# Performance work log

Hardware: AMD Instinct MI355X
Metric: run time of the kernel (lower is better)

The kernel has to match this reference:

```python
import jax, jax.numpy as jnp
import numpy as np

EPS = 1e-6
DN = ('NCHW', 'OIHW', 'NCHW')


def _dw_conv(s, w, dilation, k):
    pad = dilation * (k - 1) // 2
    return jax.lax.conv_general_dilated(
        s, w, window_strides=(1, 1), padding=[(pad, pad), (pad, pad)],
        rhs_dilation=(dilation, dilation), dimension_numbers=DN,
        feature_group_count=4)


def _branch(s, dw_w, pw_w, pw_b, dilation, k):
    h = _dw_conv(s, dw_w, dilation, k)           # [B,4,H,W]
    # pointwise 1x1 conv 4 -> 1
    return jnp.einsum('bchw,oc->bohw', h, pw_w) + pw_b[None, :, None, None]


def setup_inputs() -> dict:
    key = jax.random.key(0)
    ks = jax.random.split(key, 12)
    B, C, H, W = 32, 64, 128, 128
    nb, rh = 3, 8
    d = {}
    d['x'] = jax.random.normal(ks[0], (B, C, H, W), dtype=jnp.float32)
    # branch 0: k=3 d=1; branch 1: k=7 d=1; branch 2: k=7 d=2
    d['dw0'] = jax.random.normal(ks[1], (4, 1, 3, 3), dtype=jnp.float32) * 0.2
    d['dw1'] = jax.random.normal(ks[2], (4, 1, 7, 7), dtype=jnp.float32) * 0.1
    d['dw2'] = jax.random.normal(ks[3], (4, 1, 7, 7), dtype=jnp.float32) * 0.1
    d['pw0_w'] = jax.random.normal(ks[4], (1, 4), dtype=jnp.float32) * 0.5
    d['pw0_b'] = jnp.zeros((1,), dtype=jnp.float32)
    d['pw1_w'] = jax.random.normal(ks[5], (1, 4), dtype=jnp.float32) * 0.5
    d['pw1_b'] = jnp.zeros((1,), dtype=jnp.float32)
    d['pw2_w'] = jax.random.normal(ks[6], (1, 4), dtype=jnp.float32) * 0.5
    d['pw2_b'] = jnp.zeros((1,), dtype=jnp.float32)
    # router: 1x1 convs on pooled [B,4,1,1] == dense layers
    d['rw1'] = jax.random.normal(ks[7], (rh, 4), dtype=jnp.float32) * 0.5
    d['rb1'] = jnp.zeros((rh,), dtype=jnp.float32)
    d['rw2'] = jax.random.normal(ks[8], (nb, rh), dtype=jnp.float32) * 0.3
    d['rb2'] = jnp.zeros((nb,), dtype=jnp.float32)
    # t_raw = softplus_inverse(1.0)
    d['t_raw'] = jnp.asarray(np.log(np.expm1(1.0)), dtype=jnp.float32)
    return d


def reference(x, dw0, dw1, dw2, pw0_w, pw0_b, pw1_w, pw1_b, pw2_w, pw2_b,
              rw1, rb1, rw2, rb2, t_raw):
    B, C, H, W = x.shape
    avg_map = jnp.mean(x, axis=1, keepdims=True)        # [B,1,H,W]
    max_map = jnp.max(x, axis=1, keepdims=True)         # [B,1,H,W]
    xs = jnp.linspace(-1.0, 1.0, W, dtype=x.dtype)
    ys = jnp.linspace(-1.0, 1.0, H, dtype=x.dtype)
    yy, xx = jnp.meshgrid(ys, xs, indexing='ij')
    xg = jnp.broadcast_to(xx[None, None], (B, 1, H, W))
    yg = jnp.broadcast_to(yy[None, None], (B, 1, H, W))
    s = jnp.concatenate([avg_map, max_map, xg, yg], axis=1)  # [B,4,H,W]

    # router: global avg pool -> 1x1 conv -> relu -> 1x1 conv -> softmax
    pooled = jnp.mean(s, axis=(2, 3))                    # [B,4]
    hid = jax.nn.relu(pooled @ rw1.T + rb1)              # [B,rh]
    logits = hid @ rw2.T + rb2                           # [B,nb]
    rw = jax.nn.softmax(logits, axis=1)                  # [B,nb]

    z = jnp.stack([
        _branch(s, dw0, pw0_w, pw0_b, 1, 3),
        _branch(s, dw1, pw1_w, pw1_b, 1, 7),
        _branch(s, dw2, pw2_w, pw2_b, 2, 7),
    ], axis=1)                                           # [B,nb,1,H,W]

    wlogits = jnp.sum(rw[:, :, None, None, None] * z, axis=1)  # [B,1,H,W]
    T = jax.nn.softplus(t_raw) + EPS
    sa = jax.nn.sigmoid(wlogits / T)                     # [B,1,H,W]
    Y = x * sa                                           # [B,C,H,W]
    return (Y, sa)
```

## Files before the change

### kernel.cpp

```cpp
#include <hip/hip_runtime.h>

#define B_ 32
#define C_ 64
#define H_ 128
#define W_ 128
#define HW_ (H_*W_)
#define CHW_ (C_*HW_)

__global__ __launch_bounds__(256) void k1_reduce(
    const float* __restrict__ x, float* __restrict__ avgmap,
    float* __restrict__ maxmap, float* __restrict__ bsum)
{
    int t = blockIdx.x * 256 + threadIdx.x;
    int base = t * 4;
    int b = base >> 14;
    int q = base & (HW_ - 1);
    const float4* xp = (const float4*)(x + (size_t)b * CHW_ + q);
    float4 v = xp[0];
    float4 s = v, m = v;
    #pragma unroll 8
    for (int c = 1; c < C_; ++c) {
        float4 u = xp[c * (HW_ / 4)];
        s.x += u.x; s.y += u.y; s.z += u.z; s.w += u.w;
        m.x = fmaxf(m.x, u.x); m.y = fmaxf(m.y, u.y);
        m.z = fmaxf(m.z, u.z); m.w = fmaxf(m.w, u.w);
    }
    const float inv = 1.0f / C_;
    float4 a = make_float4(s.x * inv, s.y * inv, s.z * inv, s.w * inv);
    ((float4*)avgmap)[t] = a;
    ((float4*)maxmap)[t] = m;

    float la = a.x + a.y + a.z + a.w;
    float lm = m.x + m.y + m.z + m.w;
    #pragma unroll
    for (int o = 32; o > 0; o >>= 1) {
        la += __shfl_down(la, o);
        lm += __shfl_down(lm, o);
    }
    __shared__ float wa[4], wm[4];
    int lane = threadIdx.x & 63, wid = threadIdx.x >> 6;
    if (lane == 0) { wa[wid] = la; wm[wid] = lm; }
    __syncthreads();
    if (threadIdx.x == 0) {
        atomicAdd(&bsum[2 * b],     wa[0] + wa[1] + wa[2] + wa[3]);
        atomicAdd(&bsum[2 * b + 1], wm[0] + wm[1] + wm[2] + wm[3]);
    }
}

__global__ void k2_router(const float* __restrict__ bsum,
                          const float* __restrict__ rw1, const float* __restrict__ rb1,
                          const float* __restrict__ rw2, const float* __restrict__ rb2,
                          float* __restrict__ rwout)
{
    int b = threadIdx.x;
    if (b >= B_) return;
    float p0 = bsum[2 * b]     * (1.0f / HW_);
    float p1 = bsum[2 * b + 1] * (1.0f / HW_);
    float hid[8];
    #pragma unroll
    for (int j = 0; j < 8; ++j)
        hid[j] = fmaxf(0.0f, rb1[j] + rw1[j * 4] * p0 + rw1[j * 4 + 1] * p1);
    float lg[3];
    #pragma unroll
    for (int i = 0; i < 3; ++i) {
        float acc = rb2[i];
        #pragma unroll
        for (int j = 0; j < 8; ++j) acc += hid[j] * rw2[i * 8 + j];
        lg[i] = acc;
    }
    float mx = fmaxf(lg[0], fmaxf(lg[1], lg[2]));
    float e0 = expf(lg[0] - mx), e1 = expf(lg[1] - mx), e2 = expf(lg[2] - mx);
    float inv = 1.0f / (e0 + e1 + e2);
    rwout[b * 3 + 0] = e0 * inv;
    rwout[b * 3 + 1] = e1 * inv;
    rwout[b * 3 + 2] = e2 * inv;
}

__global__ __launch_bounds__(256) void k3_branches(
    const float* __restrict__ avgmap, const float* __restrict__ maxmap,
    const float* __restrict__ dw0, const float* __restrict__ dw1,
    const float* __restrict__ dw2,
    const float* __restrict__ pw0w, const float* __restrict__ pw0b,
    const float* __restrict__ pw1w, const float* __restrict__ pw1b,
    const float* __restrict__ pw2w, const float* __restrict__ pw2b,
    const float* __restrict__ rw, const float* __restrict__ t_raw,
    float* __restrict__ sa_out)
{
    __shared__ float sA[28][40];
    __shared__ float sM[28][40];
    __shared__ float wf0[36], wf1[196], wf2[196];

    int b = blockIdx.z;
    int tix = threadIdx.y * 16 + threadIdx.x;
    int gx0 = blockIdx.x * 16, gy0 = blockIdx.y * 16;
    const float* am = avgmap + (size_t)b * HW_;
    const float* mm = maxmap + (size_t)b * HW_;

    for (int idx = tix; idx < 28 * 28; idx += 256) {
        int r = idx / 28, c = idx % 28;
        int gy = gy0 - 6 + r, gx = gx0 - 6 + c;
        bool ok = ((unsigned)gy < H_) && ((unsigned)gx < W_);
        sA[r][c] = ok ? am[gy * W_ + gx] : 0.0f;
        sM[r][c] = ok ? mm[gy * W_ + gx] : 0.0f;
    }
    if (tix < 36)  wf0[tix] = pw0w[tix / 9]  * dw0[tix];
    if (tix < 196) {
        wf1[tix] = pw1w[tix / 49] * dw1[tix];
        wf2[tix] = pw2w[tix / 49] * dw2[tix];
    }
    __syncthreads();

    int lx = threadIdx.x, ly = threadIdx.y;
    int gx = gx0 + lx, gy = gy0 + ly;
    const float sc = 2.0f / 127.0f;

    float z0 = pw0b[0], z1 = pw1b[0], z2 = pw2b[0];

    #pragma unroll
    for (int ky = 0; ky < 3; ++ky) {
        #pragma unroll
        for (int kx = 0; kx < 3; ++kx) {
            int i = ky - 1, j = kx - 1;
            float a = sA[ly + 6 + i][lx + 6 + j];
            float m = sM[ly + 6 + i][lx + 6 + j];
            int iy = gy + i, ix = gx + j;
            bool ok = ((unsigned)iy < H_) && ((unsigned)ix < W_);
            float xv = ok ? (ix * sc - 1.0f) : 0.0f;
            float yv = ok ? (iy * sc - 1.0f) : 0.0f;
            int t = ky * 3 + kx;
            z0 += wf0[t] * a + wf0[9 + t] * m + wf0[18 + t] * xv + wf0[27 + t] * yv;
        }
    }
    #pragma unroll
    for (int ky = 0; ky < 7; ++ky) {
        #pragma unroll
        for (int kx = 0; kx < 7; ++kx) {
            int i = ky - 3, j = kx - 3;
            float a = sA[ly + 6 + i][lx + 6 + j];
            float m = sM[ly + 6 + i][lx + 6 + j];
            int iy = gy + i, ix = gx + j;
            bool ok = ((unsigned)iy < H_) && ((unsigned)ix < W_);
            float xv = ok ? (ix * sc - 1.0f) : 0.0f;
            float yv = ok ? (iy * sc - 1.0f) : 0.0f;
            int t = ky * 7 + kx;
            z1 += wf1[t] * a + wf1[49 + t] * m + wf1[98 + t] * xv + wf1[147 + t] * yv;
        }
    }
    #pragma unroll
    for (int ky = 0; ky < 7; ++ky) {
        #pragma unroll
        for (int kx = 0; kx < 7; ++kx) {
            int i = (ky - 3) * 2, j = (kx - 3) * 2;
            float a = sA[ly + 6 + i][lx + 6 + j];
            float m = sM[ly + 6 + i][lx + 6 + j];
            int iy = gy + i, ix = gx + j;
            bool ok = ((unsigned)iy < H_) && ((unsigned)ix < W_);
            float xv = ok ? (ix * sc - 1.0f) : 0.0f;
            float yv = ok ? (iy * sc - 1.0f) : 0.0f;
            int t = ky * 7 + kx;
            z2 += wf2[t] * a + wf2[49 + t] * m + wf2[98 + t] * xv + wf2[147 + t] * yv;
        }
    }

    float wl = rw[b * 3] * z0 + rw[b * 3 + 1] * z1 + rw[b * 3 + 2] * z2;
    float T = log1pf(expf(t_raw[0])) + 1e-6f;
    float s = 1.0f / (1.0f + expf(-wl / T));
    sa_out[(size_t)b * HW_ + gy * W_ + gx] = s;
}

__global__ __launch_bounds__(256) void k4_mul(
    const float* __restrict__ x, const float* __restrict__ sa,
    float* __restrict__ y)
{
    size_t t = (size_t)blockIdx.x * 256 + threadIdx.x;
    size_t base = t * 4;
    int b = (int)(base >> 20);
    int q = (int)(base & (HW_ - 1));
    float4 xv = ((const float4*)x)[t];
    float4 sv = *(const float4*)(sa + (size_t)b * HW_ + q);
    float4 yv = make_float4(xv.x * sv.x, xv.y * sv.y, xv.z * sv.z, xv.w * sv.w);
    ((float4*)y)[t] = yv;
}

extern "C" void kernel_launch(void* const* d_in, const int* in_sizes, int n_in,
                              void* d_out, int out_size, void* d_ws, size_t ws_size,
                              hipStream_t stream)
{
    const float* x     = (const float*)d_in[0];
    const float* dw0   = (const float*)d_in[1];
    const float* dw1   = (const float*)d_in[2];
    const float* dw2   = (const float*)d_in[3];
    const float* pw0w  = (const float*)d_in[4];
    const float* pw0b  = (const float*)d_in[5];
    const float* pw1w  = (const float*)d_in[6];
    const float* pw1b  = (const float*)d_in[7];
    const float* pw2w  = (const float*)d_in[8];
    const float* pw2b  = (const float*)d_in[9];
    const float* rw1   = (const float*)d_in[10];
    const float* rb1   = (const float*)d_in[11];
    const float* rw2   = (const float*)d_in[12];
    const float* rb2   = (const float*)d_in[13];
    const float* t_raw = (const float*)d_in[14];

    float* ws     = (float*)d_ws;
    float* avgmap = ws;
    float* maxmap = ws + 524288;
    float* bsum   = ws + 1048576;
    float* rw     = ws + 1048640;

    float* Y  = (float*)d_out;
    float* sa = Y + (size_t)B_ * CHW_;

    hipMemsetAsync(bsum, 0, 64 * sizeof(float), stream);

    k1_reduce<<<B_ * HW_ / 4 / 256, 256, 0, stream>>>(x, avgmap, maxmap, bsum);
    k2_router<<<1, 64, 0, stream>>>(bsum, rw1, rb1, rw2, rb2, rw);

    dim3 g3(W_ / 16, H_ / 16, B_), b3(16, 16);
    k3_branches<<<g3, b3, 0, stream>>>(avgmap, maxmap, dw0, dw1, dw2,
                                       pw0w, pw0b, pw1w, pw1b, pw2w, pw2b,
                                       rw, t_raw, sa);

    k4_mul<<<B_ * CHW_ / 4 / 256, 256, 0, stream>>>(x, sa, Y);
}
```

Before: 343.5 us.

## Fuse branch conv with gating multiply and replace atomics with per-block partials

Merges the stencil/sigmoid kernel with the x*sa multiply, so each block computes sa for two full rows and then scales all 64 channels of those rows from shared memory, avoiding a re-read of sa from global memory and one kernel launch. The tile becomes full-width 2-row strips, which allows float4 halo loads. The per-batch atomics and memset are replaced by per-block partial sums that the router reduces. The cost is that the heavy x read/write now runs in only 2048 blocks that also do conv work, which may hurt memory-level parallelism, and the 14-row halo for 2 output rows adds redundant map loads.

```diff
diff --git a/kernel.cpp b/kernel.cpp
--- a/kernel.cpp
+++ b/kernel.cpp
@@ -9,7 +9,7 @@
 
 __global__ __launch_bounds__(256) void k1_reduce(
     const float* __restrict__ x, float* __restrict__ avgmap,
-    float* __restrict__ maxmap, float* __restrict__ bsum)
+    float* __restrict__ maxmap, float* __restrict__ partial)
 {
     int t = blockIdx.x * 256 + threadIdx.x;
     int base = t * 4;
@@ -42,20 +42,26 @@
     if (lane == 0) { wa[wid] = la; wm[wid] = lm; }
     __syncthreads();
     if (threadIdx.x == 0) {
-        atomicAdd(&bsum[2 * b],     wa[0] + wa[1] + wa[2] + wa[3]);
-        atomicAdd(&bsum[2 * b + 1], wm[0] + wm[1] + wm[2] + wm[3]);
-    }
-}
-
-__global__ void k2_router(const float* __restrict__ bsum,
+        partial[2 * blockIdx.x]     = wa[0] + wa[1] + wa[2] + wa[3];
+        partial[2 * blockIdx.x + 1] = wm[0] + wm[1] + wm[2] + wm[3];
+    }
+}
+
+__global__ void k2_router(const float* __restrict__ partial,
                           const float* __restrict__ rw1, const float* __restrict__ rb1,
                           const float* __restrict__ rw2, const float* __restrict__ rb2,
                           float* __restrict__ rwout)
 {
     int b = threadIdx.x;
     if (b >= B_) return;
-    float p0 = bsum[2 * b]     * (1.0f / HW_);
-    float p1 = bsum[2 * b + 1] * (1.0f / HW_);
+    float s0 = 0.0f, s1 = 0.0f;
+    #pragma unroll
+    for (int i = 0; i < 16; ++i) {
+        s0 += partial[2 * (b * 16 + i)];
+        s1 += partial[2 * (b * 16 + i) + 1];
+    }
+    float p0 = s0 * (1.0f / HW_);
+    float p1 = s1 * (1.0f / HW_);
     float hid[8];
     #pragma unroll
     for (int j = 0; j < 8; ++j)
@@ -76,7 +82,8 @@
     rwout[b * 3 + 2] = e2 * inv;
 }
 
-__global__ __launch_bounds__(256) void k3_branches(
+__global__ __launch_bounds__(256) void k34_branches_apply(
+    const float* __restrict__ x,
     const float* __restrict__ avgmap, const float* __restrict__ maxmap,
     const float* __restrict__ dw0, const float* __restrict__ dw1,
     const float* __restrict__ dw2,
@@ -84,24 +91,37 @@
     const float* __restrict__ pw1w, const float* __restrict__ pw1b,
     const float* __restrict__ pw2w, const float* __restrict__ pw2b,
     const float* __restrict__ rw, const float* __restrict__ t_raw,
-    float* __restrict__ sa_out)
-{
-    __shared__ float sA[28][40];
-    __shared__ float sM[28][40];
+    float* __restrict__ y, float* __restrict__ sa_out)
+{
+    __shared__ float sA[14][140];
+    __shared__ float sM[14][140];
     __shared__ float wf0[36], wf1[196], wf2[196];
-
-    int b = blockIdx.z;
-    int tix = threadIdx.y * 16 + threadIdx.x;
-    int gx0 = blockIdx.x * 16, gy0 = blockIdx.y * 16;
+    __shared__ float ssa[256];
+
+    int b  = blockIdx.y;
+    int y0 = blockIdx.x * 2;
+    int tix = threadIdx.x;
     const float* am = avgmap + (size_t)b * HW_;
     const float* mm = maxmap + (size_t)b * HW_;
 
-    for (int idx = tix; idx < 28 * 28; idx += 256) {
-        int r = idx / 28, c = idx % 28;
-        int gy = gy0 - 6 + r, gx = gx0 - 6 + c;
-        bool ok = ((unsigned)gy < H_) && ((unsigned)gx < W_);
-        sA[r][c] = ok ? am[gy * W_ + gx] : 0.0f;
-        sM[r][c] = ok ? mm[gy * W_ + gx] : 0.0f;
+    for (int idx = tix; idx < 14 * 32; idx += 256) {
+        int r = idx >> 5, c4 = idx & 31;
+        int gy = y0 - 6 + r;
+        bool ok = (unsigned)gy < H_;
+        float4 av = ok ? ((const float4*)(am + gy * W_))[c4]
+                       : make_float4(0.f, 0.f, 0.f, 0.f);
+        float4 mv = ok ? ((const float4*)(mm + gy * W_))[c4]
+                       : make_float4(0.f, 0.f, 0.f, 0.f);
+        float* pa = &sA[r][6 + c4 * 4];
+        float* pm = &sM[r][6 + c4 * 4];
+        pa[0] = av.x; pa[1] = av.y; pa[2] = av.z; pa[3] = av.w;
+        pm[0] = mv.x; pm[1] = mv.y; pm[2] = mv.z; pm[3] = mv.w;
+    }
+    for (int idx = tix; idx < 14 * 12; idx += 256) {
+        int r = idx / 12, c = idx % 12;
+        int cc = (c < 6) ? c : (134 + c - 6);
+        sA[r][cc] = 0.0f;
+        sM[r][cc] = 0.0f;
     }
     if (tix < 36)  wf0[tix] = pw0w[tix / 9]  * dw0[tix];
     if (tix < 196) {
@@ -110,9 +130,11 @@
     }
     __syncthreads();
 
-    int lx = threadIdx.x, ly = threadIdx.y;
-    int gx = gx0 + lx, gy = gy0 + ly;
+    int ly = tix >> 7;
+    int lx = tix & 127;
+    int gy = y0 + ly;
     const float sc = 2.0f / 127.0f;
+    const float xv_c = lx * sc - 1.0f;
 
     float z0 = pw0b[0], z1 = pw1b[0], z2 = pw2b[0];
 
@@ -123,7 +145,7 @@
             int i = ky - 1, j = kx - 1;
             float a = sA[ly + 6 + i][lx + 6 + j];
             float m = sM[ly + 6 + i][lx + 6 + j];
-            int iy = gy + i, ix = gx + j;
+            int iy = gy + i, ix = lx + j;
             bool ok = ((unsigned)iy < H_) && ((unsigned)ix < W_);
             float xv = ok ? (ix * sc - 1.0f) : 0.0f;
             float yv = ok ? (iy * sc - 1.0f) : 0.0f;
@@ -138,7 +160,7 @@
             int i = ky - 3, j = kx - 3;
             float a = sA[ly + 6 + i][lx + 6 + j];
             float m = sM[ly + 6 + i][lx + 6 + j];
-            int iy = gy + i, ix = gx + j;
+            int iy = gy + i, ix = lx + j;
             bool ok = ((unsigned)iy < H_) && ((unsigned)ix < W_);
             float xv = ok ? (ix * sc - 1.0f) : 0.0f;
             float yv = ok ? (iy * sc - 1.0f) : 0.0f;
@@ -153,7 +175,7 @@
             int i = (ky - 3) * 2, j = (kx - 3) * 2;
             float a = sA[ly + 6 + i][lx + 6 + j];
             float m = sM[ly + 6 + i][lx + 6 + j];
-            int iy = gy + i, ix = gx + j;
+            int iy = gy + i, ix = lx + j;
             bool ok = ((unsigned)iy < H_) && ((unsigned)ix < W_);
             float xv = ok ? (ix * sc - 1.0f) : 0.0f;
             float yv = ok ? (iy * sc - 1.0f) : 0.0f;
@@ -165,21 +187,23 @@
     float wl = rw[b * 3] * z0 + rw[b * 3 + 1] * z1 + rw[b * 3 + 2] * z2;
     float T = log1pf(expf(t_raw[0])) + 1e-6f;
     float s = 1.0f / (1.0f + expf(-wl / T));
-    sa_out[(size_t)b * HW_ + gy * W_ + gx] = s;
-}
-
-__global__ __launch_bounds__(256) void k4_mul(
-    const float* __restrict__ x, const float* __restrict__ sa,
-    float* __restrict__ y)
-{
-    size_t t = (size_t)blockIdx.x * 256 + threadIdx.x;
-    size_t base = t * 4;
-    int b = (int)(base >> 20);
-    int q = (int)(base & (HW_ - 1));
-    float4 xv = ((const float4*)x)[t];
-    float4 sv = *(const float4*)(sa + (size_t)b * HW_ + q);
-    float4 yv = make_float4(xv.x * sv.x, xv.y * sv.y, xv.z * sv.z, xv.w * sv.w);
-    ((float4*)y)[t] = yv;
+    ssa[tix] = s;
+    sa_out[(size_t)b * HW_ + gy * W_ + lx] = s;
+    __syncthreads();
+
+    int wid  = tix >> 6;
+    int lane = tix & 63;
+    float4 sv = ((const float4*)ssa)[lane];
+    const float* xt = x + (size_t)b * CHW_ + y0 * W_;
+    float*       yt = y + (size_t)b * CHW_ + y0 * W_;
+    #pragma unroll 4
+    for (int k = 0; k < 16; ++k) {
+        int c = wid + k * 4;
+        float4 xv4 = ((const float4*)(xt + c * HW_))[lane];
+        float4 yv4 = make_float4(xv4.x * sv.x, xv4.y * sv.y,
+                                 xv4.z * sv.z, xv4.w * sv.w);
+        ((float4*)(yt + c * HW_))[lane] = yv4;
+    }
 }
 
 extern "C" void kernel_launch(void* const* d_in, const int* in_sizes, int n_in,
@@ -202,24 +226,21 @@
     const float* rb2   = (const float*)d_in[13];
     const float* t_raw = (const float*)d_in[14];
 
-    float* ws     = (float*)d_ws;
-    float* avgmap = ws;
-    float* maxmap = ws + 524288;
-    float* bsum   = ws + 1048576;
-    float* rw     = ws + 1048640;
+    float* ws      = (float*)d_ws;
+    float* avgmap  = ws;
+    float* maxmap  = ws + 524288;
+    float* partial = ws + 1048576;
+    float* rw      = ws + 1049600;
 
     float* Y  = (float*)d_out;
     float* sa = Y + (size_t)B_ * CHW_;
 
-    hipMemsetAsync(bsum, 0, 64 * sizeof(float), stream);
-
-    k1_reduce<<<B_ * HW_ / 4 / 256, 256, 0, stream>>>(x, avgmap, maxmap, bsum);
-    k2_router<<<1, 64, 0, stream>>>(bsum, rw1, rb1, rw2, rb2, rw);
-
-    dim3 g3(W_ / 16, H_ / 16, B_), b3(16, 16);
-    k3_branches<<<g3, b3, 0, stream>>>(avgmap, maxmap, dw0, dw1, dw2,
-                                       pw0w, pw0b, pw1w, pw1b, pw2w, pw2b,
-                                       rw, t_raw, sa);
-
-    k4_mul<<<B_ * CHW_ / 4 / 256, 256, 0, stream>>>(x, sa, Y);
-}
+    k1_reduce<<<B_ * HW_ / 4 / 256, 256, 0, stream>>>(x, avgmap, maxmap, partial);
+    k2_router<<<1, 64, 0, stream>>>(partial, rw1, rb1, rw2, rb2, rw);
+
+    dim3 g34(H_ / 2, B_);
+    k34_branches_apply<<<g34, 256, 0, stream>>>(
+        x, avgmap, maxmap, dw0, dw1, dw2,
+        pw0w, pw0b, pw1w, pw1b, pw2w, pw2b,
+        rw, t_raw, Y, sa);
+}
```

Result: faster. 307.9 us (-10.4%).
